# Kernel tuning notes

Hardware: AMD Instinct MI355X
Metric: run time of the kernel (lower is better)

The kernel has to match this reference:

```python
import jax, jax.numpy as jnp
import numpy as np

B = 100        # number of queries
N = 50000      # n_node
E = 600000     # n_edges
D = 128        # in_dim = out_dim (hidden_dim)
A = 64         # attn_dim
R = 200        # n_rel -> rela_embed has 2*R+1 = 401 rows


def setup_inputs() -> dict:
    key = jax.random.key(0)
    ks = jax.random.split(key, 14)
    q_sub = jax.random.randint(ks[0], (B,), 0, N)
    q_rel = jax.random.randint(ks[1], (B,), 0, 2 * R + 1)
    # edges: [E, 6]; col0=r_idx(<B), col2=rel(<2R+1), col4=sub(<N), col5=obj(<N); cols 1,3 unused
    c0 = jax.random.randint(ks[2], (E,), 0, B)
    c2 = jax.random.randint(ks[3], (E,), 0, 2 * R + 1)
    c4 = jax.random.randint(ks[4], (E,), 0, N)
    c5 = jax.random.randint(ks[5], (E,), 0, N)
    z = jnp.zeros((E,), dtype=jnp.int32)
    edges = jnp.stack([c0, z, c2, z, c4, c5], axis=1)
    hidden = jax.random.normal(ks[6], (N, D), dtype=jnp.float32)
    # learned parameters
    rela_embed = jax.random.normal(ks[7], (2 * R + 1, D), dtype=jnp.float32) * 0.02
    Ws = jax.random.normal(ks[8], (D, A), dtype=jnp.float32) * 0.05   # Ws_attn.weight^T
    Wr = jax.random.normal(ks[9], (D, A), dtype=jnp.float32) * 0.05   # Wr_attn.weight^T
    Wqr = jax.random.normal(ks[10], (D, A), dtype=jnp.float32) * 0.05 # Wqr_attn.weight^T
    bqr = jnp.zeros((A,), dtype=jnp.float32)
    wa = jax.random.normal(ks[11], (A, 1), dtype=jnp.float32) * 0.05  # w_alpha.weight^T
    ba = jnp.zeros((1,), dtype=jnp.float32)
    Wh = jax.random.normal(ks[12], (D, D), dtype=jnp.float32) * 0.05  # W_h.weight^T
    return {"q_sub": q_sub, "q_rel": q_rel, "hidden": hidden, "edges": edges,
            "n_node": N, "rela_embed": rela_embed, "Ws": Ws, "Wr": Wr,
            "Wqr": Wqr, "bqr": bqr, "wa": wa, "ba": ba, "Wh": Wh}


def reference(q_sub, q_rel, hidden, edges, n_node, rela_embed, Ws, Wr, Wqr, bqr, wa, ba, Wh):
    sub = edges[:, 4]
    rel = edges[:, 2]
    obj = edges[:, 5]
    r_idx = edges[:, 0]
    hs = hidden[sub]                       # [E, D] gather
    hr = rela_embed[rel]                   # [E, D] gather
    h_qr = rela_embed[q_rel][r_idx]        # [B, D] then gather -> [E, D]
    # attention score per edge
    pre = hs @ Ws + hr @ Wr + h_qr @ Wqr + bqr          # [E, A]
    alpha = jax.nn.sigmoid(jax.nn.relu(pre) @ wa + ba)   # [E, 1]
    message = alpha * (hs + hr)                          # [E, D]
    message_agg = jax.ops.segment_sum(message, obj, num_segments=n_node)  # [N, D]
    hidden_new = message_agg @ Wh                        # act = identity ('idd')
    return hidden_new
```

## Files before the change

kernel.cpp:

```cpp
#include <hip/hip_runtime.h>

#define DD 128
#define AA 64
#define SS 96

static inline int idiv_up(int a, int b) { return (a + b - 1) / b; }

__device__ __forceinline__ unsigned short f2bf(float f) {
    unsigned u = __float_as_uint(f);
    u += 0x7fff + ((u >> 16) & 1);
    return (unsigned short)(u >> 16);
}
__device__ __forceinline__ float bf2f(unsigned short h) {
    return __uint_as_float(((unsigned)h) << 16);
}

__global__ __launch_bounds__(256)
void proj_all_kernel(const float* __restrict__ hidden,
                     const float* __restrict__ rela,
                     const int* __restrict__ q_rel,
                     const float* __restrict__ Ws,
                     const float* __restrict__ Wr,
                     const float* __restrict__ Wqr,
                     const float* __restrict__ bqr,
                     const float* __restrict__ Wh,
                     float* __restrict__ subrows,
                     float* __restrict__ hrWr,
                     float* __restrict__ relaWh,
                     float* __restrict__ hqrWqr,
                     int N, int NR, int B, int nA, int nB) {
    __shared__ float lht[128 * 64];
    const int t = threadIdx.x;
    const int bid = blockIdx.x;
    int type, rbase, nrows;
    const float* src;
    if (bid < nA)           { type = 0; rbase = bid * 64;             nrows = N;  src = hidden; }
    else if (bid < nA + nB) { type = 1; rbase = (bid - nA) * 64;      nrows = NR; src = rela; }
    else                    { type = 2; rbase = (bid - nA - nB) * 64; nrows = B;  src = rela; }

    const int row = t & 63;
    const int d0 = (t >> 6) * 32;
    const int gr = rbase + row;
    const float* srow = nullptr;
    if (gr < nrows) {
        const int sr = (type == 2) ? q_rel[gr] : gr;
        srow = src + (long)sr * DD;
    }
    #pragma unroll
    for (int j = 0; j < 8; ++j) {
        float4 v = make_float4(0.f, 0.f, 0.f, 0.f);
        if (srow) v = *(const float4*)&srow[d0 + j * 4];
        lht[(d0 + j * 4 + 0) * 64 + row] = v.x;
        lht[(d0 + j * 4 + 1) * 64 + row] = v.y;
        lht[(d0 + j * 4 + 2) * 64 + row] = v.z;
        lht[(d0 + j * 4 + 3) * 64 + row] = v.w;
    }
    __syncthreads();

    const int r0 = (t & 15) * 4;
    const int c0 = (t >> 4) * 4;

    const float* W0 = ((type == 0) ? Ws : (type == 1) ? Wr : Wqr) + c0;
    const float* W1 = Wh + c0;
    const float* W2 = Wh + 64 + c0;

    float acc[4][12] = {};
    #pragma unroll 4
    for (int d = 0; d < 128; ++d) {
        const float4 hv  = *(const float4*)&lht[d * 64 + r0];
        const float4 wv0 = *(const float4*)&W0[(long)d * 64];
        const float4 wv1 = *(const float4*)&W1[(long)d * 128];
        const float4 wv2 = *(const float4*)&W2[(long)d * 128];
        const float h[4] = { hv.x, hv.y, hv.z, hv.w };
        #pragma unroll
        for (int i = 0; i < 4; ++i) {
            acc[i][0]  = fmaf(h[i], wv0.x, acc[i][0]);
            acc[i][1]  = fmaf(h[i], wv0.y, acc[i][1]);
            acc[i][2]  = fmaf(h[i], wv0.z, acc[i][2]);
            acc[i][3]  = fmaf(h[i], wv0.w, acc[i][3]);
            acc[i][4]  = fmaf(h[i], wv1.x, acc[i][4]);
            acc[i][5]  = fmaf(h[i], wv1.y, acc[i][5]);
            acc[i][6]  = fmaf(h[i], wv1.z, acc[i][6]);
            acc[i][7]  = fmaf(h[i], wv1.w, acc[i][7]);
            acc[i][8]  = fmaf(h[i], wv2.x, acc[i][8]);
            acc[i][9]  = fmaf(h[i], wv2.y, acc[i][9]);
            acc[i][10] = fmaf(h[i], wv2.z, acc[i][10]);
            acc[i][11] = fmaf(h[i], wv2.w, acc[i][11]);
        }
    }

    #pragma unroll
    for (int i = 0; i < 4; ++i) {
        const int orow = rbase + r0 + i;
        if (orow >= nrows) continue;
        if (type == 0) {
            float* srw = subrows + (long)orow * SS;
            ushort4 o0, o1, o2;
            o0.x = f2bf(acc[i][0]);  o0.y = f2bf(acc[i][1]);
            o0.z = f2bf(acc[i][2]);  o0.w = f2bf(acc[i][3]);
            o1.x = f2bf(acc[i][4]);  o1.y = f2bf(acc[i][5]);
            o1.z = f2bf(acc[i][6]);  o1.w = f2bf(acc[i][7]);
            o2.x = f2bf(acc[i][8]);  o2.y = f2bf(acc[i][9]);
            o2.z = f2bf(acc[i][10]); o2.w = f2bf(acc[i][11]);
            *(ushort4*)((unsigned short*)srw + c0) = o0;
            *(ushort4*)((unsigned short*)(srw + 32) + c0) = o1;
            *(ushort4*)((unsigned short*)(srw + 32) + 64 + c0) = o2;
        } else if (type == 1) {
            *(float4*)&hrWr[(long)orow * 64 + c0] =
                make_float4(acc[i][0], acc[i][1], acc[i][2], acc[i][3]);
            *(float4*)&relaWh[(long)orow * 128 + c0] =
                make_float4(acc[i][4], acc[i][5], acc[i][6], acc[i][7]);
            *(float4*)&relaWh[(long)orow * 128 + 64 + c0] =
                make_float4(acc[i][8], acc[i][9], acc[i][10], acc[i][11]);
        } else {
            const float4 bq = *(const float4*)&bqr[c0];
            *(float4*)&hqrWqr[(long)orow * 64 + c0] =
                make_float4(acc[i][0] + bq.x, acc[i][1] + bq.y,
                            acc[i][2] + bq.z, acc[i][3] + bq.w);
        }
    }
}

__global__ void hist_kernel(const int* __restrict__ edges, int* deg, int E) {
    const int e0 = (blockIdx.x * blockDim.x + threadIdx.x) * 4;
    if (e0 >= E) return;
    if (e0 + 3 < E) {
        const int4* p = (const int4*)&edges[(long)e0 * 6];
        const int4 j1 = p[1], j2 = p[2], j4 = p[4], j5 = p[5];
        atomicAdd(&deg[j1.y], 1);
        atomicAdd(&deg[j2.w], 1);
        atomicAdd(&deg[j4.y], 1);
        atomicAdd(&deg[j5.w], 1);
    } else {
        for (int e = e0; e < E; ++e) atomicAdd(&deg[edges[(long)e * 6 + 5]], 1);
    }
}

__global__ __launch_bounds__(256)
void scan_kernel(const int* __restrict__ deg, int* __restrict__ loff,
                 int* __restrict__ cur, int* __restrict__ bsum,
                 int* __restrict__ bsumx, int* __restrict__ done,
                 int n, int nb) {
    __shared__ int tsum[256];
    __shared__ int lastFlag;
    const int t = threadIdx.x;
    const int b = blockIdx.x;
    const int base = b * 1024 + t * 4;
    int v[4];
    int s = 0;
    #pragma unroll
    for (int j = 0; j < 4; ++j) {
        v[j] = (base + j < n) ? deg[base + j] : 0;
        s += v[j];
    }
    tsum[t] = s;
    __syncthreads();
    for (int o = 1; o < 256; o <<= 1) {
        const int x = (t >= o) ? tsum[t - o] : 0;
        __syncthreads();
        tsum[t] += x;
        __syncthreads();
    }
    int run = (t > 0) ? tsum[t - 1] : 0;
    #pragma unroll
    for (int j = 0; j < 4; ++j) {
        if (base + j < n) { loff[base + j] = run; cur[base + j] = run; }
        run += v[j];
    }
    if (t == 255) {
        bsum[b] = tsum[255];
        __threadfence();
    }
    __syncthreads();
    if (t == 0) lastFlag = (atomicAdd(done, 1) == nb - 1);
    __syncthreads();
    if (lastFlag && t < 64) {
        __threadfence();
        const int val = (t < nb) ? bsum[t] : 0;
        int inc = val;
        #pragma unroll
        for (int o = 1; o < 64; o <<= 1) {
            const int x = __shfl_up(inc, o, 64);
            if (t >= o) inc += x;
        }
        if (t < nb) bsumx[t] = inc - val;
    }
}

__global__ void scatter_kernel(const int* __restrict__ edges, int* cur,
                               const int* __restrict__ bsumx,
                               int2* __restrict__ recs, int E) {
    const int e0 = (blockIdx.x * blockDim.x + threadIdx.x) * 4;
    if (e0 >= E) return;
    if (e0 + 3 < E) {
        const int4* p = (const int4*)&edges[(long)e0 * 6];
        const int4 j0 = p[0], j1 = p[1], j2 = p[2], j3 = p[3], j4 = p[4], j5 = p[5];
        {
            const int pos = bsumx[j1.y >> 10] + atomicAdd(&cur[j1.y], 1);
            recs[pos] = make_int2(j1.x, j0.z | (j0.x << 16));
        }
        {
            const int pos = bsumx[j2.w >> 10] + atomicAdd(&cur[j2.w], 1);
            recs[pos] = make_int2(j2.z, j2.x | (j1.z << 16));
        }
        {
            const int pos = bsumx[j4.y >> 10] + atomicAdd(&cur[j4.y], 1);
            recs[pos] = make_int2(j4.x, j3.z | (j3.x << 16));
        }
        {
            const int pos = bsumx[j5.w >> 10] + atomicAdd(&cur[j5.w], 1);
            recs[pos] = make_int2(j5.z, j5.x | (j4.z << 16));
        }
    } else {
        for (int e = e0; e < E; ++e) {
            const int* ed = edges + (long)e * 6;
            const int obj = ed[5];
            const int pos = bsumx[obj >> 10] + atomicAdd(&cur[obj], 1);
            recs[pos] = make_int2(ed[4], ed[2] | (ed[0] << 16));
        }
    }
}

__global__ __launch_bounds__(256)
void gather_kernel(const int2* __restrict__ recs,
                   const int* __restrict__ loff,
                   const int* __restrict__ bsumx,
                   const float* __restrict__ subrows,
                   const float* __restrict__ hrWr,
                   const float* __restrict__ hqrWqr,
                   const float* __restrict__ relaWh,
                   const float* __restrict__ wa,
                   const float* __restrict__ ba,
                   float* __restrict__ out, int N, int E) {
    const int lane = threadIdx.x & 63;
    const int g = lane >> 4;
    const int l = lane & 15;
    const int v = (int)((blockIdx.x * blockDim.x + threadIdx.x) >> 6);
    if (v >= N) return;
    const float4 wav = *(const float4*)&wa[l * 4];
    const float bar = ba[0];
    const int start = loff[v] + bsumx[v >> 10];
    const int end = (v + 1 < N) ? (loff[v + 1] + bsumx[(v + 1) >> 10]) : E;

    float4 acc0 = make_float4(0.f, 0.f, 0.f, 0.f);
    float4 acc1 = make_float4(0.f, 0.f, 0.f, 0.f);

    for (int base = start; base < end; base += 8) {
        const int k1 = base + g;
        const int k2 = base + 4 + g;
        const bool va1 = (k1 < end);
        const bool va2 = (k2 < end);
        const int2 rc1 = va1 ? recs[k1] : make_int2(0, 0);
        const int2 rc2 = va2 ? recs[k2] : make_int2(0, 0);
        const int sub1 = rc1.x, rel1 = rc1.y & 0xffff, rid1 = rc1.y >> 16;
        const int sub2 = rc2.x, rel2 = rc2.y & 0xffff, rid2 = rc2.y >> 16;
        const float* sr1 = subrows + (long)sub1 * SS;
        const float* sr2 = subrows + (long)sub2 * SS;

        const ushort4 hw1 = *(const ushort4*)((const unsigned short*)sr1 + l * 4);
        const ushort4 hw2 = *(const ushort4*)((const unsigned short*)sr2 + l * 4);
        const float4 b41 = *(const float4*)&hrWr[rel1 * AA + l * 4];
        const float4 b42 = *(const float4*)&hrWr[rel2 * AA + l * 4];
        const float4 c41 = *(const float4*)&hqrWqr[rid1 * AA + l * 4];
        const float4 c42 = *(const float4*)&hqrWqr[rid2 * AA + l * 4];
        const ushort4 m01 = *(const ushort4*)((const unsigned short*)(sr1 + 32) + l * 8);
        const ushort4 m11 = *(const ushort4*)((const unsigned short*)(sr1 + 32) + l * 8 + 4);
        const ushort4 m02 = *(const ushort4*)((const unsigned short*)(sr2 + 32) + l * 8);
        const ushort4 m12 = *(const ushort4*)((const unsigned short*)(sr2 + 32) + l * 8 + 4);
        const float4 r01 = *(const float4*)&relaWh[rel1 * DD + l * 8];
        const float4 r11 = *(const float4*)&relaWh[rel1 * DD + l * 8 + 4];
        const float4 r02 = *(const float4*)&relaWh[rel2 * DD + l * 8];
        const float4 r12 = *(const float4*)&relaWh[rel2 * DD + l * 8 + 4];

        float s1 = fmaxf(bf2f(hw1.x) + b41.x + c41.x, 0.f) * wav.x;
        s1 = fmaf(fmaxf(bf2f(hw1.y) + b41.y + c41.y, 0.f), wav.y, s1);
        s1 = fmaf(fmaxf(bf2f(hw1.z) + b41.z + c41.z, 0.f), wav.z, s1);
        s1 = fmaf(fmaxf(bf2f(hw1.w) + b41.w + c41.w, 0.f), wav.w, s1);
        float s2 = fmaxf(bf2f(hw2.x) + b42.x + c42.x, 0.f) * wav.x;
        s2 = fmaf(fmaxf(bf2f(hw2.y) + b42.y + c42.y, 0.f), wav.y, s2);
        s2 = fmaf(fmaxf(bf2f(hw2.z) + b42.z + c42.z, 0.f), wav.z, s2);
        s2 = fmaf(fmaxf(bf2f(hw2.w) + b42.w + c42.w, 0.f), wav.w, s2);
        s1 += __shfl_xor(s1, 1);  s2 += __shfl_xor(s2, 1);
        s1 += __shfl_xor(s1, 2);  s2 += __shfl_xor(s2, 2);
        s1 += __shfl_xor(s1, 4);  s2 += __shfl_xor(s2, 4);
        s1 += __shfl_xor(s1, 8);  s2 += __shfl_xor(s2, 8);
        float al1 = __builtin_amdgcn_rcpf(1.0f + __expf(-(s1 + bar)));
        float al2 = __builtin_amdgcn_rcpf(1.0f + __expf(-(s2 + bar)));
        if (!va1) al1 = 0.0f;
        if (!va2) al2 = 0.0f;

        acc0.x = fmaf(al1, bf2f(m01.x) + r01.x, acc0.x);
        acc0.y = fmaf(al1, bf2f(m01.y) + r01.y, acc0.y);
        acc0.z = fmaf(al1, bf2f(m01.z) + r01.z, acc0.z);
        acc0.w = fmaf(al1, bf2f(m01.w) + r01.w, acc0.w);
        acc1.x = fmaf(al1, bf2f(m11.x) + r11.x, acc1.x);
        acc1.y = fmaf(al1, bf2f(m11.y) + r11.y, acc1.y);
        acc1.z = fmaf(al1, bf2f(m11.z) + r11.z, acc1.z);
        acc1.w = fmaf(al1, bf2f(m11.w) + r11.w, acc1.w);
        acc0.x = fmaf(al2, bf2f(m02.x) + r02.x, acc0.x);
        acc0.y = fmaf(al2, bf2f(m02.y) + r02.y, acc0.y);
        acc0.z = fmaf(al2, bf2f(m02.z) + r02.z, acc0.z);
        acc0.w = fmaf(al2, bf2f(m02.w) + r02.w, acc0.w);
        acc1.x = fmaf(al2, bf2f(m12.x) + r12.x, acc1.x);
        acc1.y = fmaf(al2, bf2f(m12.y) + r12.y, acc1.y);
        acc1.z = fmaf(al2, bf2f(m12.z) + r12.z, acc1.z);
        acc1.w = fmaf(al2, bf2f(m12.w) + r12.w, acc1.w);
    }

    #pragma unroll
    for (int o = 16; o <= 32; o <<= 1) {
        acc0.x += __shfl_xor(acc0.x, o);
        acc0.y += __shfl_xor(acc0.y, o);
        acc0.z += __shfl_xor(acc0.z, o);
        acc0.w += __shfl_xor(acc0.w, o);
        acc1.x += __shfl_xor(acc1.x, o);
        acc1.y += __shfl_xor(acc1.y, o);
        acc1.z += __shfl_xor(acc1.z, o);
        acc1.w += __shfl_xor(acc1.w, o);
    }
    if (g == 0) {
        *(float4*)&out[(long)v * DD + l * 8]     = acc0;
        *(float4*)&out[(long)v * DD + l * 8 + 4] = acc1;
    }
}

extern "C" void kernel_launch(void* const* d_in, const int* in_sizes, int n_in,
                              void* d_out, int out_size, void* d_ws, size_t ws_size,
                              hipStream_t stream) {
    const int*   q_rel  = (const int*)d_in[1];
    const float* hidden = (const float*)d_in[2];
    const int*   edges  = (const int*)d_in[3];
    const float* rela   = (const float*)d_in[5];
    const float* Ws     = (const float*)d_in[6];
    const float* Wr     = (const float*)d_in[7];
    const float* Wqr    = (const float*)d_in[8];
    const float* bqr    = (const float*)d_in[9];
    const float* wa     = (const float*)d_in[10];
    const float* ba     = (const float*)d_in[11];
    const float* Wh     = (const float*)d_in[12];

    const int B  = in_sizes[1];
    const int N  = in_sizes[2] / DD;
    const int E  = in_sizes[3] / 6;
    const int NR = in_sizes[5] / DD;

    float* out = (float*)d_out;

    float* subrows = (float*)d_ws;
    float* hrWr    = subrows + (size_t)N * SS;
    float* relaWh  = hrWr + (size_t)NR * AA;
    float* hqrWqr  = relaWh + (size_t)NR * DD;
    int*   deg     = (int*)(hqrWqr + (size_t)B * AA);
    int*   done    = deg + N;
    int*   cur     = done + 3;
    int*   loff    = cur + N;
    int*   bsum    = loff + N;
    int*   bsumx   = bsum + 64;
    int2*  recs    = (int2*)(bsumx + 64);

    const int nA = idiv_up(N, 64);
    const int nB = idiv_up(NR, 64);
    const int nC = idiv_up(B, 64);
    const int nb = idiv_up(N, 1024);

    hipMemsetAsync(deg, 0, (size_t)(N + 1) * sizeof(int), stream);
    proj_all_kernel<<<nA + nB + nC, 256, 0, stream>>>(
        hidden, rela, q_rel, Ws, Wr, Wqr, bqr, Wh,
        subrows, hrWr, relaWh, hqrWqr, N, NR, B, nA, nB);
    hist_kernel<<<idiv_up(E, 1024), 256, 0, stream>>>(edges, deg, E);
    scan_kernel<<<nb, 256, 0, stream>>>(deg, loff, cur, bsum, bsumx, done, N, nb);
    scatter_kernel<<<idiv_up(E, 1024), 256, 0, stream>>>(edges, cur, bsumx, recs, E);
    gather_kernel<<<idiv_up(N * 64, 256), 256, 0, stream>>>(
        recs, loff, bsumx, subrows, hrWr, hqrWqr, relaWh, wa, ba, out, N, E);
}
```

Before: 290.4 us.

## Fuse degree histogram into projection kernel and split output columns across blocks

Merges the edge-degree histogram into the projection launch as extra tail blocks, removing one kernel launch and letting the atomic counting overlap with the GEMM work. The projection now splits its three 64-column output slices into separate blocks, each staging its weight slice in shared memory instead of reading weights from global memory every iteration. This triples the number of hidden-row tiles loaded and transposed, and doubles shared memory per block to 64 KB, which may lower occupancy.

Measured after the change: 257.2 us. 11.4% less time.

```diff
diff --git a/kernel.cpp b/kernel.cpp
--- a/kernel.cpp
+++ b/kernel.cpp
@@ -16,27 +16,66 @@
 }
 
 __global__ __launch_bounds__(256)
-void proj_all_kernel(const float* __restrict__ hidden,
-                     const float* __restrict__ rela,
-                     const int* __restrict__ q_rel,
-                     const float* __restrict__ Ws,
-                     const float* __restrict__ Wr,
-                     const float* __restrict__ Wqr,
-                     const float* __restrict__ bqr,
-                     const float* __restrict__ Wh,
-                     float* __restrict__ subrows,
-                     float* __restrict__ hrWr,
-                     float* __restrict__ relaWh,
-                     float* __restrict__ hqrWqr,
-                     int N, int NR, int B, int nA, int nB) {
+void proj_hist_kernel(const float* __restrict__ hidden,
+                      const float* __restrict__ rela,
+                      const int* __restrict__ q_rel,
+                      const float* __restrict__ Ws,
+                      const float* __restrict__ Wr,
+                      const float* __restrict__ Wqr,
+                      const float* __restrict__ bqr,
+                      const float* __restrict__ Wh,
+                      const int* __restrict__ edges,
+                      int* __restrict__ deg,
+                      float* __restrict__ subrows,
+                      float* __restrict__ hrWr,
+                      float* __restrict__ relaWh,
+                      float* __restrict__ hqrWqr,
+                      int N, int NR, int B, int E,
+                      int nA, int nB, int nC) {
     __shared__ float lht[128 * 64];
+    __shared__ float wslice[128 * 64];
     const int t = threadIdx.x;
     const int bid = blockIdx.x;
-    int type, rbase, nrows;
+    const int nP = 3 * nA + 3 * nB + nC;
+
+    if (bid >= nP) {
+        const int base = (bid - nP) * 4096;
+        #pragma unroll
+        for (int k = 0; k < 4; ++k) {
+            const int e0 = base + (k * 256 + t) * 4;
+            if (e0 >= E) break;
+            if (e0 + 3 < E) {
+                const int4* p = (const int4*)&edges[(long)e0 * 6];
+                const int4 j1 = p[1], j2 = p[2], j4 = p[4], j5 = p[5];
+                atomicAdd(&deg[j1.y], 1);
+                atomicAdd(&deg[j2.w], 1);
+                atomicAdd(&deg[j4.y], 1);
+                atomicAdd(&deg[j5.w], 1);
+            } else {
+                for (int e = e0; e < E; ++e) atomicAdd(&deg[edges[(long)e * 6 + 5]], 1);
+            }
+        }
+        return;
+    }
+
+    int type, tile, s, nrows;
     const float* src;
-    if (bid < nA)           { type = 0; rbase = bid * 64;             nrows = N;  src = hidden; }
-    else if (bid < nA + nB) { type = 1; rbase = (bid - nA) * 64;      nrows = NR; src = rela; }
-    else                    { type = 2; rbase = (bid - nA - nB) * 64; nrows = B;  src = rela; }
+    if (bid < 3 * nA)           { type = 0; tile = bid / 3;            s = bid - tile * 3;       nrows = N;  src = hidden; }
+    else if (bid < 3 * (nA+nB)) { const int pb = bid - 3 * nA; type = 1; tile = pb / 3; s = pb - tile * 3; nrows = NR; src = rela; }
+    else                        { type = 2; tile = bid - 3 * (nA+nB);  s = 0;                    nrows = B;  src = rela; }
+    const int rbase = tile * 64;
+
+    const float* W;
+    int ldw, off;
+    if (s == 0) { W = (type == 0) ? Ws : (type == 1) ? Wr : Wqr; ldw = 64;  off = 0; }
+    else if (s == 1) { W = Wh; ldw = 128; off = 0; }
+    else             { W = Wh; ldw = 128; off = 64; }
+
+    #pragma unroll
+    for (int k = 0; k < 8192; k += 1024) {
+        const int f = k + t * 4;
+        *(float4*)&wslice[f] = *(const float4*)&W[(long)(f >> 6) * ldw + off + (f & 63)];
+    }
 
     const int row = t & 63;
     const int d0 = (t >> 6) * 32;
@@ -60,33 +99,27 @@
     const int r0 = (t & 15) * 4;
     const int c0 = (t >> 4) * 4;
 
-    const float* W0 = ((type == 0) ? Ws : (type == 1) ? Wr : Wqr) + c0;
-    const float* W1 = Wh + c0;
-    const float* W2 = Wh + 64 + c0;
-
-    float acc[4][12] = {};
+    float acc[4][4] = {};
     #pragma unroll 4
     for (int d = 0; d < 128; ++d) {
-        const float4 hv  = *(const float4*)&lht[d * 64 + r0];
-        const float4 wv0 = *(const float4*)&W0[(long)d * 64];
-        const float4 wv1 = *(const float4*)&W1[(long)d * 128];
-        const float4 wv2 = *(const float4*)&W2[(long)d * 128];
-        const float h[4] = { hv.x, hv.y, hv.z, hv.w };
-        #pragma unroll
-        for (int i = 0; i < 4; ++i) {
-            acc[i][0]  = fmaf(h[i], wv0.x, acc[i][0]);
-            acc[i][1]  = fmaf(h[i], wv0.y, acc[i][1]);
-            acc[i][2]  = fmaf(h[i], wv0.z, acc[i][2]);
-            acc[i][3]  = fmaf(h[i], wv0.w, acc[i][3]);
-            acc[i][4]  = fmaf(h[i], wv1.x, acc[i][4]);
-            acc[i][5]  = fmaf(h[i], wv1.y, acc[i][5]);
-            acc[i][6]  = fmaf(h[i], wv1.z, acc[i][6]);
-            acc[i][7]  = fmaf(h[i], wv1.w, acc[i][7]);
-            acc[i][8]  = fmaf(h[i], wv2.x, acc[i][8]);
-            acc[i][9]  = fmaf(h[i], wv2.y, acc[i][9]);
-            acc[i][10] = fmaf(h[i], wv2.z, acc[i][10]);
-            acc[i][11] = fmaf(h[i], wv2.w, acc[i][11]);
-        }
+        const float4 hv = *(const float4*)&lht[d * 64 + r0];
+        const float4 wv = *(const float4*)&wslice[d * 64 + c0];
+        acc[0][0] = fmaf(hv.x, wv.x, acc[0][0]);
+        acc[0][1] = fmaf(hv.x, wv.y, acc[0][1]);
+        acc[0][2] = fmaf(hv.x, wv.z, acc[0][2]);
+        acc[0][3] = fmaf(hv.x, wv.w, acc[0][3]);
+        acc[1][0] = fmaf(hv.y, wv.x, acc[1][0]);
+        acc[1][1] = fmaf(hv.y, wv.y, acc[1][1]);
+        acc[1][2] = fmaf(hv.y, wv.z, acc[1][2]);
+        acc[1][3] = fmaf(hv.y, wv.w, acc[1][3]);
+        acc[2][0] = fmaf(hv.z, wv.x, acc[2][0]);
+        acc[2][1] = fmaf(hv.z, wv.y, acc[2][1]);
+        acc[2][2] = fmaf(hv.z, wv.z, acc[2][2]);
+        acc[2][3] = fmaf(hv.z, wv.w, acc[2][3]);
+        acc[3][0] = fmaf(hv.w, wv.x, acc[3][0]);
+        acc[3][1] = fmaf(hv.w, wv.y, acc[3][1]);
+        acc[3][2] = fmaf(hv.w, wv.z, acc[3][2]);
+        acc[3][3] = fmaf(hv.w, wv.w, acc[3][3]);
     }
 
     #pragma unroll
@@ -95,44 +128,23 @@
         if (orow >= nrows) continue;
         if (type == 0) {
             float* srw = subrows + (long)orow * SS;
-            ushort4 o0, o1, o2;
-            o0.x = f2bf(acc[i][0]);  o0.y = f2bf(acc[i][1]);
-            o0.z = f2bf(acc[i][2]);  o0.w = f2bf(acc[i][3]);
-            o1.x = f2bf(acc[i][4]);  o1.y = f2bf(acc[i][5]);
-            o1.z = f2bf(acc[i][6]);  o1.w = f2bf(acc[i][7]);
-            o2.x = f2bf(acc[i][8]);  o2.y = f2bf(acc[i][9]);
-            o2.z = f2bf(acc[i][10]); o2.w = f2bf(acc[i][11]);
-            *(ushort4*)((unsigned short*)srw + c0) = o0;
-            *(ushort4*)((unsigned short*)(srw + 32) + c0) = o1;
-            *(ushort4*)((unsigned short*)(srw + 32) + 64 + c0) = o2;
+            ushort4 o;
+            o.x = f2bf(acc[i][0]); o.y = f2bf(acc[i][1]);
+            o.z = f2bf(acc[i][2]); o.w = f2bf(acc[i][3]);
+            if (s == 0)      *(ushort4*)((unsigned short*)srw + c0) = o;
+            else if (s == 1) *(ushort4*)((unsigned short*)(srw + 32) + c0) = o;
+            else             *(ushort4*)((unsigned short*)(srw + 32) + 64 + c0) = o;
         } else if (type == 1) {
-            *(float4*)&hrWr[(long)orow * 64 + c0] =
-                make_float4(acc[i][0], acc[i][1], acc[i][2], acc[i][3]);
-            *(float4*)&relaWh[(long)orow * 128 + c0] =
-                make_float4(acc[i][4], acc[i][5], acc[i][6], acc[i][7]);
-            *(float4*)&relaWh[(long)orow * 128 + 64 + c0] =
-                make_float4(acc[i][8], acc[i][9], acc[i][10], acc[i][11]);
+            const float4 o = make_float4(acc[i][0], acc[i][1], acc[i][2], acc[i][3]);
+            if (s == 0)      *(float4*)&hrWr[(long)orow * 64 + c0] = o;
+            else if (s == 1) *(float4*)&relaWh[(long)orow * 128 + c0] = o;
+            else             *(float4*)&relaWh[(long)orow * 128 + 64 + c0] = o;
         } else {
             const float4 bq = *(const float4*)&bqr[c0];
             *(float4*)&hqrWqr[(long)orow * 64 + c0] =
                 make_float4(acc[i][0] + bq.x, acc[i][1] + bq.y,
                             acc[i][2] + bq.z, acc[i][3] + bq.w);
         }
-    }
-}
-
-__global__ void hist_kernel(const int* __restrict__ edges, int* deg, int E) {
-    const int e0 = (blockIdx.x * blockDim.x + threadIdx.x) * 4;
-    if (e0 >= E) return;
-    if (e0 + 3 < E) {
-        const int4* p = (const int4*)&edges[(long)e0 * 6];
-        const int4 j1 = p[1], j2 = p[2], j4 = p[4], j5 = p[5];
-        atomicAdd(&deg[j1.y], 1);
-        atomicAdd(&deg[j2.w], 1);
-        atomicAdd(&deg[j4.y], 1);
-        atomicAdd(&deg[j5.w], 1);
-    } else {
-        for (int e = e0; e < E; ++e) atomicAdd(&deg[edges[(long)e * 6 + 5]], 1);
     }
 }
 
@@ -361,13 +373,14 @@
     const int nA = idiv_up(N, 64);
     const int nB = idiv_up(NR, 64);
     const int nC = idiv_up(B, 64);
+    const int nH = idiv_up(E, 4096);
     const int nb = idiv_up(N, 1024);
+    const int grid_ph = 3 * nA + 3 * nB + nC + nH;
 
     hipMemsetAsync(deg, 0, (size_t)(N + 1) * sizeof(int), stream);
-    proj_all_kernel<<<nA + nB + nC, 256, 0, stream>>>(
-        hidden, rela, q_rel, Ws, Wr, Wqr, bqr, Wh,
-        subrows, hrWr, relaWh, hqrWqr, N, NR, B, nA, nB);
-    hist_kernel<<<idiv_up(E, 1024), 256, 0, stream>>>(edges, deg, E);
+    proj_hist_kernel<<<grid_ph, 256, 0, stream>>>(
+        hidden, rela, q_rel, Ws, Wr, Wqr, bqr, Wh, edges, deg,
+        subrows, hrWr, relaWh, hqrWqr, N, NR, B, E, nA, nB, nC);
     scan_kernel<<<nb, 256, 0, stream>>>(deg, loff, cur, bsum, bsumx, done, N, nb);
     scatter_kernel<<<idiv_up(E, 1024), 256, 0, stream>>>(edges, cur, bsumx, recs, E);
     gather_kernel<<<idiv_up(N * 64, 256), 256, 0, stream>>>(
```
